# Kernel tuning notes

Measured on AMD Instinct MI355X. Metric: run time of the kernel, lower is better.

Reference implementation:

```python
import jax, jax.numpy as jnp
import numpy as np

N_COUNTIES = 3144
P = 2
N_MOB = 6
N_COV = 10
T = 156
NNZ = 31440


def setup_inputs() -> dict:
    key = jax.random.key(0)
    ks = jax.random.split(key, 13)
    C = jax.random.uniform(ks[0], (T, N_COUNTIES), dtype=jnp.float32)
    D = jax.random.uniform(ks[1], (T, N_COUNTIES), dtype=jnp.float32)
    M = jax.random.uniform(ks[2], (N_MOB, T, N_COUNTIES), dtype=jnp.float32)
    cov = jax.random.normal(ks[3], (N_COV, N_COUNTIES), dtype=jnp.float32)
    B_nonzero = jax.random.normal(ks[4], (NNZ,), dtype=jnp.float32)
    A_nonzero = jax.random.normal(ks[5], (NNZ,), dtype=jnp.float32)
    H_nonzero = jax.random.normal(ks[6], (NNZ,), dtype=jnp.float32)
    mu = jax.random.normal(ks[7], (N_MOB, P), dtype=jnp.float32)
    nu = jax.random.normal(ks[8], (N_MOB, P), dtype=jnp.float32)
    upsilon = jax.random.normal(ks[9], (N_COV,), dtype=jnp.float32)
    zeta = jax.random.normal(ks[10], (N_COV,), dtype=jnp.float32)
    rows = jax.random.randint(ks[11], (NNZ,), 0, N_COUNTIES)
    cols = jax.random.randint(ks[12], (NNZ,), 0, N_COUNTIES)
    return dict(C=C, D=D, M=M, cov=cov, B_nonzero=B_nonzero, A_nonzero=A_nonzero,
                H_nonzero=H_nonzero, mu=mu, nu=nu, upsilon=upsilon, zeta=zeta,
                rows=rows, cols=cols)


def reference(C, D, M, cov, B_nonzero, A_nonzero, H_nonzero, mu, nu, upsilon, zeta, rows, cols):
    n = C.shape[1]
    p = mu.shape[1]
    Tp = C.shape[0] - p  # number of predicted steps (t = p .. T-1)

    # Dense scatter-built weight matrices (duplicates summed, matching
    # torch.sparse .to_dense()). The torch code reuses the SAME nonzero
    # vector for every lag tau, so B[tau] == B for all tau.
    B = jnp.zeros((n, n), C.dtype).at[rows, cols].add(B_nonzero)
    A = jnp.zeros((n, n), C.dtype).at[rows, cols].add(A_nonzero)
    H = jnp.zeros((n, n), C.dtype).at[rows, cols].add(H_nonzero)

    # Lagged windows: Cl[tau, i] = C[i + tau] == C[t - p + tau] for t = p + i.
    Cl = jnp.stack([C[tau:tau + Tp] for tau in range(p)], 0)  # [p, Tp, n]
    Dl = jnp.stack([D[tau:tau + Tp] for tau in range(p)], 0)  # [p, Tp, n]
    Ml = jnp.stack([M[:, tau:tau + Tp, :] for tau in range(p)], 1)  # [n_mob, p, Tp, n]

    # Since B[tau] are identical across lags, sum over p folds into one GEMM.
    c2c = jnp.einsum('ptn,nm->tm', Cl, B)  # [Tp, n]
    c2d = jnp.einsum('ptn,nm->tm', Cl, H)
    d2d = jnp.einsum('ptn,nm->tm', Dl, A)

    mob_c = jnp.einsum('kptn,kp->tn', Ml, mu)
    mob_d = jnp.einsum('kptn,kp->tn', Ml, nu)

    C_hat = c2c + mob_c + upsilon @ cov  # [Tp, n] (+ broadcast [n])
    D_hat = c2d + d2d + mob_d + zeta @ cov
    return C_hat, D_hat
```

## Files before the change

kernel.cpp:

```cpp
#include <hip/hip_runtime.h>


#define BS      256
#define ECAP    64
#define SPILLC  4096
#define SCAN_TH 1024
#define POISON  0xAAAAAAAAu

__global__ void prep(const int* __restrict__ rows, const int* __restrict__ cols,
                     const float* __restrict__ Bnz, const float* __restrict__ Anz,
                     const float* __restrict__ Hnz,
                     const float* __restrict__ C, const float* __restrict__ D,
                     float2* __restrict__ CsDs,
                     float4* __restrict__ edges, unsigned* __restrict__ cnt,
                     unsigned* __restrict__ spill_cnt, int* __restrict__ spill,
                     int T, int NC, int NNZ, int TPn, int fillBlocks, int tT64) {
    if ((int)blockIdx.x < fillBlocks) {
        int k = blockIdx.x * BS + threadIdx.x;
        if (k < NNZ) {
            int c = cols[k];
            unsigned j = atomicAdd(&cnt[c], 1u) - POISON;
            if (j < ECAP)
                edges[(size_t)c * ECAP + j] =
                    make_float4(__int_as_float(rows[k]), Bnz[k], Anz[k], Hnz[k]);
            else {
                unsigned sp = atomicAdd(spill_cnt, 1u) - POISON;
                if (sp < SPILLC) spill[sp] = k;
            }
        }
        return;
    }
    __shared__ float tc[65][65], td[65][65];
    int bid = blockIdx.x - fillBlocks;
    int ct = bid / tT64, tt = bid - ct * tT64;
    int lx = threadIdx.x & 63, ly = threadIdx.x >> 6;
    int c0 = ct * 64, t0 = tt * 64;
    for (int rr = ly; rr < 65; rr += 4) {
        int t = t0 + rr, c = c0 + lx;
        if (t < T && c < NC) {
            tc[rr][lx] = C[(size_t)t * NC + c];
            td[rr][lx] = D[(size_t)t * NC + c];
        }
    }
    __syncthreads();
    for (int rr = ly; rr < 64; rr += 4) {
        int c = c0 + rr, t = t0 + lx;
        if (c < NC && t < TPn)
            CsDs[(size_t)c * TPn + t] =
                make_float2(tc[lx][rr] + tc[lx + 1][rr],
                            td[lx][rr] + td[lx + 1][rr]);
    }
}

__global__ void mega(const float2* __restrict__ CsDs,
                     const unsigned* __restrict__ cnt, const float4* __restrict__ edges,
                     const float* __restrict__ M,
                     const float* __restrict__ cov,
                     const float* __restrict__ mu,
                     const float* __restrict__ nu,
                     const float* __restrict__ ups, const float* __restrict__ zet,
                     const int* __restrict__ rows, const int* __restrict__ cols,
                     const float* __restrict__ Bnz, const float* __restrict__ Anz,
                     const float* __restrict__ Hnz,
                     const unsigned* __restrict__ spill_cnt, const int* __restrict__ spill,
                     float* __restrict__ out0, float* __restrict__ out1,
                     int T, int NC, int TPn) {
    int c = blockIdx.x * blockDim.x + threadIdx.x;
    if (c >= NC) return;
    int i0 = (int)blockIdx.y * 2;

    unsigned n = cnt[c] - POISON;
    if (n > ECAP) n = ECAP;
    const float4* eb = edges + (size_t)c * ECAP;
    float s00 = 0.f, s01 = 0.f, s10 = 0.f, s11 = 0.f;
    for (unsigned j = 0; j < n; ++j) {
        float4 E = eb[j];
        int g = __float_as_int(E.x);
        float4 v = *(const float4*)(CsDs + (size_t)g * TPn + i0);
        s00 += v.x * E.y;
        s01 += v.x * E.w + v.y * E.z;
        s10 += v.z * E.y;
        s11 += v.z * E.w + v.w * E.z;
    }

    float cv0 = 0.f, cv1 = 0.f;
#pragma unroll
    for (int j = 0; j < 10; ++j) {
        float cv = cov[(size_t)j * NC + c];
        cv0 += cv * ups[j];
        cv1 += cv * zet[j];
    }
    float a00 = s00 + cv0, a01 = s01 + cv1;
    float a10 = s10 + cv0, a11 = s11 + cv1;

#pragma unroll
    for (int k = 0; k < 6; ++k) {
        const float* Mk = M + (size_t)(k * T + i0) * NC + c;
        float m0 = Mk[0];
        float m1 = Mk[(size_t)NC];
        float m2 = Mk[(size_t)2 * NC];
        float u0 = mu[k * 2], u1 = mu[k * 2 + 1];
        float w0 = nu[k * 2], w1 = nu[k * 2 + 1];
        a00 += m0 * u0 + m1 * u1;
        a01 += m0 * w0 + m1 * w1;
        a10 += m1 * u0 + m2 * u1;
        a11 += m1 * w0 + m2 * w1;
    }

    unsigned nsp = *spill_cnt - POISON;
    if (nsp != 0) {
        if (nsp > SPILLC) nsp = SPILLC;
        for (unsigned s = 0; s < nsp; ++s) {
            int k = spill[s];
            if (cols[k] == c) {
                int g = rows[k];
                float4 v = *(const float4*)(CsDs + (size_t)g * TPn + i0);
                a00 += v.x * Bnz[k];
                a01 += v.x * Hnz[k] + v.y * Anz[k];
                a10 += v.z * Bnz[k];
                a11 += v.z * Hnz[k] + v.w * Anz[k];
            }
        }
    }

    out0[(size_t)i0 * NC + c] = a00;
    out1[(size_t)i0 * NC + c] = a01;
    out0[(size_t)(i0 + 1) * NC + c] = a10;
    out1[(size_t)(i0 + 1) * NC + c] = a11;
}

__global__ void csr_hist(const int* __restrict__ cols, int* __restrict__ counts, int NNZ) {
    int k = blockIdx.x * blockDim.x + threadIdx.x;
    if (k < NNZ) atomicAdd(&counts[cols[k]], 1);
}
__global__ __launch_bounds__(SCAN_TH)
void csr_scan(const int* __restrict__ counts, int* __restrict__ offsets,
              int* __restrict__ cursor, int NC) {
    __shared__ int ssum[SCAN_TH];
    int t = threadIdx.x;
    int chunk = (NC + SCAN_TH - 1) / SCAN_TH;
    int beg = t * chunk, end = min(beg + chunk, NC);
    int local = 0;
    for (int j = beg; j < end; ++j) local += counts[j];
    ssum[t] = local;
    __syncthreads();
    for (int off = 1; off < SCAN_TH; off <<= 1) {
        int v = (t >= off) ? ssum[t - off] : 0;
        __syncthreads();
        ssum[t] += v;
        __syncthreads();
    }
    int run = ssum[t] - local;
    for (int j = beg; j < end; ++j) {
        offsets[j] = run;
        cursor[j]  = run;
        run += counts[j];
    }
    if (t == SCAN_TH - 1) offsets[NC] = ssum[SCAN_TH - 1];
}
__global__ void csr_fill(const int* __restrict__ rows, const int* __restrict__ cols,
                         const float* __restrict__ Bnz, const float* __restrict__ Anz,
                         const float* __restrict__ Hnz,
                         int* __restrict__ cursor, float4* __restrict__ edges, int NNZ) {
    int k = blockIdx.x * blockDim.x + threadIdx.x;
    if (k >= NNZ) return;
    int s = cols[k];
    int pos = atomicAdd(&cursor[s], 1);
    edges[pos] = make_float4(__int_as_float(rows[k]), Bnz[k], Anz[k], Hnz[k]);
}
__global__ void fused_generic(const float* __restrict__ C, const float* __restrict__ D,
                              const float* __restrict__ M, const float* __restrict__ cov,
                              const float* __restrict__ mu, const float* __restrict__ nu,
                              const float* __restrict__ ups, const float* __restrict__ zet,
                              const int* __restrict__ offsets, const float4* __restrict__ edges,
                              float* __restrict__ out0, float* __restrict__ out1,
                              int T, int NC, int NMOB, int NCOV, int P, int TPn) {
    int idx = blockIdx.x * blockDim.x + threadIdx.x;
    if (idx >= TPn * NC) return;
    int i = idx / NC;
    int c = idx - i * NC;
    float acc0 = 0.f, acc1 = 0.f;
    for (int k = 0; k < NMOB; ++k)
        for (int tau = 0; tau < P; ++tau) {
            float m = M[((size_t)k * T + i + tau) * NC + c];
            acc0 += m * mu[k * P + tau];
            acc1 += m * nu[k * P + tau];
        }
    for (int j = 0; j < NCOV; ++j) {
        float cv = cov[(size_t)j * NC + c];
        acc0 += cv * ups[j];
        acc1 += cv * zet[j];
    }
    int e0 = offsets[c], e1 = offsets[c + 1];
    for (int e = e0; e < e1; ++e) {
        float4 E = edges[e];
        int g = __float_as_int(E.x);
        float cs = 0.f, ds = 0.f;
        for (int tau = 0; tau < P; ++tau) {
            cs += C[(size_t)(i + tau) * NC + g];
            ds += D[(size_t)(i + tau) * NC + g];
        }
        acc0 += cs * E.y;
        acc1 += cs * E.w + ds * E.z;
    }
    out0[idx] = acc0;
    out1[idx] = acc1;
}

extern "C" void kernel_launch(void* const* d_in, const int* in_sizes, int n_in,
                              void* d_out, int out_size, void* d_ws, size_t ws_size,
                              hipStream_t stream) {
    const float* C    = (const float*)d_in[0];
    const float* D    = (const float*)d_in[1];
    const float* M    = (const float*)d_in[2];
    const float* cov  = (const float*)d_in[3];
    const float* Bnz  = (const float*)d_in[4];
    const float* Anz  = (const float*)d_in[5];
    const float* Hnz  = (const float*)d_in[6];
    const float* mu   = (const float*)d_in[7];
    const float* nu   = (const float*)d_in[8];
    const float* ups  = (const float*)d_in[9];
    const float* zet  = (const float*)d_in[10];
    const int*  rows  = (const int*)d_in[11];
    const int*  cols  = (const int*)d_in[12];

    int NCOV = in_sizes[9];
    int NC   = in_sizes[3] / NCOV;
    int T    = in_sizes[0] / NC;
    int NMOB = in_sizes[2] / in_sizes[0];
    int P    = in_sizes[7] / NMOB;
    int NNZ  = in_sizes[11];
    int TPn  = T - P;

    float* out0 = (float*)d_out;
    float* out1 = out0 + (size_t)TPn * NC;

    float4*   edges  = (float4*)d_ws;
    unsigned* cnt    = (unsigned*)(edges + (size_t)NC * ECAP);
    unsigned* spillc = cnt + NC;
    int*      spill  = (int*)(spillc + 1);
    uintptr_t pa     = (uintptr_t)(spill + SPILLC);
    pa               = (pa + 15) & ~(uintptr_t)15;
    float2*   CsDs   = (float2*)pa;
    size_t    need   = (size_t)((char*)(CsDs + (size_t)NC * TPn) - (char*)d_ws);

    if (P == 2 && NMOB == 6 && NCOV == 10 && TPn > 0 && (TPn & 1) == 0 &&
        ws_size >= need) {
        int fillBlocks = (NNZ + BS - 1) / BS;
        int cT64 = (NC + 63) / 64, tT64 = (T + 63) / 64;
        prep<<<fillBlocks + cT64 * tT64, BS, 0, stream>>>(
            rows, cols, Bnz, Anz, Hnz, C, D, CsDs,
            edges, cnt, spillc, spill, T, NC, NNZ, TPn, fillBlocks, tT64);

        dim3 mg((NC + BS - 1) / BS, TPn / 2);
        mega<<<mg, BS, 0, stream>>>(
            CsDs, cnt, edges, M, cov, mu, nu, ups, zet,
            rows, cols, Bnz, Anz, Hnz, spillc, spill,
            out0, out1, T, NC, TPn);
    } else {
        float4* fedges   = (float4*)d_ws;
        int*    foffsets = (int*)(fedges + NNZ);
        int*    fcounts  = foffsets + (NC + 1);
        int*    fcursor  = fcounts + NC;
        hipMemsetAsync(fcounts, 0, (size_t)NC * sizeof(int), stream);
        csr_hist<<<(NNZ + BS - 1) / BS, BS, 0, stream>>>(cols, fcounts, NNZ);
        csr_scan<<<1, SCAN_TH, 0, stream>>>(fcounts, foffsets, fcursor, NC);
        csr_fill<<<(NNZ + BS - 1) / BS, BS, 0, stream>>>(
            rows, cols, Bnz, Anz, Hnz, fcursor, fedges, NNZ);
        int n = TPn * NC;
        fused_generic<<<(n + BS - 1) / BS, BS, 0, stream>>>(
            C, D, M, cov, mu, nu, ups, zet, foffsets, fedges,
            out0, out1, T, NC, NMOB, NCOV, P, TPn);
    }
}
```

Baseline: 127.5 us.

## Map wavefronts to columns with time-lane gathers and transpose via LDS

The main kernel now assigns one wavefront per destination column, with its 64 lanes covering consecutive time steps. Each edge then becomes a uniform edge-list read plus a coalesced contiguous read of CsDs along time, replacing scattered per-thread gathers across random rows. Partial sums are transposed through shared memory so the mobility, covariate and output phase keeps coalesced access along columns. In exchange each thread computes one time step instead of two, so the pairing reuse of M loads is lost, and the GC=8 column grouping can leave the last time chunk partly idle.

```diff
diff --git a/kernel.cpp b/kernel.cpp
--- a/kernel.cpp
+++ b/kernel.cpp
@@ -6,6 +6,7 @@
 #define SPILLC  4096
 #define SCAN_TH 1024
 #define POISON  0xAAAAAAAAu
+#define GC      8
 
 __global__ void prep(const int* __restrict__ rows, const int* __restrict__ cols,
                      const float* __restrict__ Bnz, const float* __restrict__ Anz,
@@ -52,37 +53,52 @@
     }
 }
 
-__global__ void mega(const float2* __restrict__ CsDs,
-                     const unsigned* __restrict__ cnt, const float4* __restrict__ edges,
-                     const float* __restrict__ M,
-                     const float* __restrict__ cov,
-                     const float* __restrict__ mu,
-                     const float* __restrict__ nu,
-                     const float* __restrict__ ups, const float* __restrict__ zet,
-                     const int* __restrict__ rows, const int* __restrict__ cols,
-                     const float* __restrict__ Bnz, const float* __restrict__ Anz,
-                     const float* __restrict__ Hnz,
-                     const unsigned* __restrict__ spill_cnt, const int* __restrict__ spill,
-                     float* __restrict__ out0, float* __restrict__ out1,
-                     int T, int NC, int TPn) {
-    int c = blockIdx.x * blockDim.x + threadIdx.x;
-    if (c >= NC) return;
-    int i0 = (int)blockIdx.y * 2;
-
-    unsigned n = cnt[c] - POISON;
-    if (n > ECAP) n = ECAP;
-    const float4* eb = edges + (size_t)c * ECAP;
-    float s00 = 0.f, s01 = 0.f, s10 = 0.f, s11 = 0.f;
-    for (unsigned j = 0; j < n; ++j) {
-        float4 E = eb[j];
-        int g = __float_as_int(E.x);
-        float4 v = *(const float4*)(CsDs + (size_t)g * TPn + i0);
-        s00 += v.x * E.y;
-        s01 += v.x * E.w + v.y * E.z;
-        s10 += v.z * E.y;
-        s11 += v.z * E.w + v.w * E.z;
-    }
-
+__global__ __launch_bounds__(64 * GC)
+void sparse_final(const float2* __restrict__ CsDs,
+                  const unsigned* __restrict__ cnt, const float4* __restrict__ edges,
+                  const float* __restrict__ M,
+                  const float* __restrict__ cov,
+                  const float* __restrict__ mu,
+                  const float* __restrict__ nu,
+                  const float* __restrict__ ups, const float* __restrict__ zet,
+                  const int* __restrict__ rows, const int* __restrict__ cols,
+                  const float* __restrict__ Bnz, const float* __restrict__ Anz,
+                  const float* __restrict__ Hnz,
+                  const unsigned* __restrict__ spill_cnt, const int* __restrict__ spill,
+                  float* __restrict__ out0, float* __restrict__ out1,
+                  int T, int NC, int TPn) {
+    __shared__ float2 sh[64][GC + 1];
+    int w    = threadIdx.x >> 6;
+    int lane = threadIdx.x & 63;
+    int cA   = blockIdx.x * GC + w;
+    int iA   = (int)blockIdx.y * 64 + lane;
+
+    float a0 = 0.f, a1 = 0.f;
+    if (cA < NC) {
+        int cu = __builtin_amdgcn_readfirstlane(cA);
+        bool valid = iA < TPn;
+        int isafe = valid ? iA : (TPn - 1);
+        unsigned n = cnt[cu] - POISON;
+        if (n > ECAP) n = ECAP;
+        const float4* eb = edges + (size_t)cu * ECAP;
+        for (unsigned j = 0; j < n; ++j) {
+            float4 E = eb[j];
+            int g = __float_as_int(E.x);
+            float2 v = CsDs[(size_t)g * TPn + isafe];
+            a0 += v.x * E.y;
+            a1 += v.x * E.w + v.y * E.z;
+        }
+    }
+    sh[lane][w] = make_float2(a0, a1);
+    __syncthreads();
+
+    int ip = threadIdx.x >> 3;
+    int cp = threadIdx.x & 7;
+    int c = blockIdx.x * GC + cp;
+    int i = (int)blockIdx.y * 64 + ip;
+    if (c >= NC || i >= TPn) return;
+
+    float2 s = sh[ip][cp];
     float cv0 = 0.f, cv1 = 0.f;
 #pragma unroll
     for (int j = 0; j < 10; ++j) {
@@ -90,43 +106,32 @@
         cv0 += cv * ups[j];
         cv1 += cv * zet[j];
     }
-    float a00 = s00 + cv0, a01 = s01 + cv1;
-    float a10 = s10 + cv0, a11 = s11 + cv1;
-
+    float A0 = s.x + cv0, A1 = s.y + cv1;
 #pragma unroll
     for (int k = 0; k < 6; ++k) {
-        const float* Mk = M + (size_t)(k * T + i0) * NC + c;
+        const float* Mk = M + ((size_t)(k * T + i)) * NC + c;
         float m0 = Mk[0];
         float m1 = Mk[(size_t)NC];
-        float m2 = Mk[(size_t)2 * NC];
-        float u0 = mu[k * 2], u1 = mu[k * 2 + 1];
-        float w0 = nu[k * 2], w1 = nu[k * 2 + 1];
-        a00 += m0 * u0 + m1 * u1;
-        a01 += m0 * w0 + m1 * w1;
-        a10 += m1 * u0 + m2 * u1;
-        a11 += m1 * w0 + m2 * w1;
+        A0 += m0 * mu[k * 2] + m1 * mu[k * 2 + 1];
+        A1 += m0 * nu[k * 2] + m1 * nu[k * 2 + 1];
     }
 
     unsigned nsp = *spill_cnt - POISON;
-    if (nsp != 0) {
+    if (__builtin_expect(nsp != 0, 0)) {
         if (nsp > SPILLC) nsp = SPILLC;
-        for (unsigned s = 0; s < nsp; ++s) {
-            int k = spill[s];
+        for (unsigned sidx = 0; sidx < nsp; ++sidx) {
+            int k = spill[sidx];
             if (cols[k] == c) {
                 int g = rows[k];
-                float4 v = *(const float4*)(CsDs + (size_t)g * TPn + i0);
-                a00 += v.x * Bnz[k];
-                a01 += v.x * Hnz[k] + v.y * Anz[k];
-                a10 += v.z * Bnz[k];
-                a11 += v.z * Hnz[k] + v.w * Anz[k];
+                float2 v = CsDs[(size_t)g * TPn + i];
+                A0 += v.x * Bnz[k];
+                A1 += v.x * Hnz[k] + v.y * Anz[k];
             }
         }
     }
 
-    out0[(size_t)i0 * NC + c] = a00;
-    out1[(size_t)i0 * NC + c] = a01;
-    out0[(size_t)(i0 + 1) * NC + c] = a10;
-    out1[(size_t)(i0 + 1) * NC + c] = a11;
+    out0[(size_t)i * NC + c] = A0;
+    out1[(size_t)i * NC + c] = A1;
 }
 
 __global__ void csr_hist(const int* __restrict__ cols, int* __restrict__ counts, int NNZ) {
@@ -244,16 +249,16 @@
     float2*   CsDs   = (float2*)pa;
     size_t    need   = (size_t)((char*)(CsDs + (size_t)NC * TPn) - (char*)d_ws);
 
-    if (P == 2 && NMOB == 6 && NCOV == 10 && TPn > 0 && (TPn & 1) == 0 &&
-        ws_size >= need) {
+    if (P == 2 && NMOB == 6 && NCOV == 10 && TPn > 0 && ws_size >= need) {
         int fillBlocks = (NNZ + BS - 1) / BS;
         int cT64 = (NC + 63) / 64, tT64 = (T + 63) / 64;
         prep<<<fillBlocks + cT64 * tT64, BS, 0, stream>>>(
             rows, cols, Bnz, Anz, Hnz, C, D, CsDs,
             edges, cnt, spillc, spill, T, NC, NNZ, TPn, fillBlocks, tT64);
 
-        dim3 mg((NC + BS - 1) / BS, TPn / 2);
-        mega<<<mg, BS, 0, stream>>>(
+        int nChunks = (TPn + 63) / 64;
+        dim3 grid((NC + GC - 1) / GC, nChunks);
+        sparse_final<<<grid, 64 * GC, 0, stream>>>(
             CsDs, cnt, edges, M, cov, mu, nu, ups, zet,
             rows, cols, Bnz, Anz, Hnz, spillc, spill,
             out0, out1, T, NC, TPn);
```

Measured after the change: 116.4 us. -8.7%, faster.
